# Performance work log

Hardware: AMD Instinct MI355X
Metric: run time of the kernel (lower is better)

Reference implementation:

```python
import jax, jax.numpy as jnp
import numpy as np

N_NODES = 100000
N_EDGES = 1600000
IN_DIM, HIDDEN, OUT = 256, 128, 64


def setup_inputs() -> dict:
    key = jax.random.key(0)
    k1, k2, k3, k4 = jax.random.split(key, 4)
    x = jax.random.normal(k1, (N_NODES, IN_DIM), dtype=jnp.float32)
    edge_index = jax.random.randint(k2, (2, N_EDGES), 0, N_NODES, dtype=jnp.int32)
    # glorot-ish init for the GCN linear layers
    W1 = jax.random.normal(k3, (IN_DIM, HIDDEN), dtype=jnp.float32) / np.sqrt(IN_DIM)
    b1 = jnp.zeros((HIDDEN,), dtype=jnp.float32)
    W2 = jax.random.normal(k4, (HIDDEN, OUT), dtype=jnp.float32) / np.sqrt(HIDDEN)
    b2 = jnp.zeros((OUT,), dtype=jnp.float32)
    return {"x": x, "edge_index": edge_index, "W1": W1, "b1": b1, "W2": W2, "b2": b2}


def gcn_layer(x, src, dst, W, b):
    """PyG GCNConv: add self-loops, symmetric deg^-1/2 normalization,
    linear transform, scatter-add aggregation, bias."""
    h = x @ W  # [N, F_out]
    # degree over self-looped graph: in-degree(dst counts) + 1 self loop
    deg = jax.ops.segment_sum(jnp.ones((src.shape[0],), h.dtype), dst,
                              num_segments=N_NODES) + 1.0
    dinv = jax.lax.rsqrt(deg)  # [N]
    coef = dinv[src] * dinv[dst]  # [E]
    agg = jax.ops.segment_sum(h[src] * coef[:, None], dst, num_segments=N_NODES)
    # self-loop contribution (norm = dinv[i]^2) without materializing loop edges
    agg = agg + h * (dinv * dinv)[:, None]
    return agg + b


def reference(x, edge_index, W1, b1, W2, b2):
    src, dst = edge_index[0], edge_index[1]
    h = jax.nn.relu(gcn_layer(x, src, dst, W1, b1))
    return jax.nn.relu(gcn_layer(h, src, dst, W2, b2))
```

## Files before the change

kernel.cpp:

```cpp
#include <hip/hip_runtime.h>

#define N_NODES 100000
#define N_EDGES 1600000
#define IN_DIM 256
#define HIDDEN 128
#define OUT_DIM 64

#define NBIN 391
#define NBLK3 256
#define CHUNK 6250
#define NMAT (NBIN * NBLK3)
#define NBLK_SCAN (NMAT / 256)
#define CAP 6144

#define G1_TILES 782
#define G_HIST  160
#define G_SCAN1 120
#define G_SCAN2 60
#define G_SCAT  160
#define G_FINE  282
#define OFF_HIST  0
#define OFF_SCAN1 160
#define OFF_SCAN2 280
#define OFF_SCAT  340
#define OFF_FINE  500

#define CAPL1 640
#define CAPL2 1024

typedef __bf16 bf16x8 __attribute__((ext_vector_type(8)));
typedef __bf16 bf16x4 __attribute__((ext_vector_type(4)));
typedef float f32x4 __attribute__((ext_vector_type(4)));

__device__ __forceinline__ int bsw1h(int c, int kk) {
    return c * 128 + (kk ^ ((c & 7) << 3));
}

__device__ __forceinline__ void gemm1_tile(const float* __restrict__ X,
                                           const float* __restrict__ W1,
                                           __bf16* __restrict__ H,
                                           int bid, __bf16* Bs) {
    const int t = threadIdx.x;
    const int wave = t >> 6;
    const int lane = t & 63;
    const int lm = lane & 15;
    const int q = lane >> 4;
    const int row0 = bid * 128;
    const int g = row0 + wave * 16 + lm;

    f32x4 acc[8] = {};

    for (int half = 0; half < 2; ++half) {
        __syncthreads();
        for (int p = 0; p < 4; ++p) {
            int i = t + 512 * p;
            int c = i & 127;
            int kg = i >> 7;
            float v[8];
            #pragma unroll
            for (int j = 0; j < 8; ++j)
                v[j] = W1[(half * 128 + kg * 8 + j) * HIDDEN + c];
            bf16x8 w;
            #pragma unroll
            for (int j = 0; j < 8; ++j) w[j] = (__bf16)v[j];
            *(bf16x8*)&Bs[bsw1h(c, kg * 8)] = w;
        }
        __syncthreads();

        #pragma unroll
        for (int k0 = 0; k0 < 128; k0 += 32) {
            float4 v0 = make_float4(0.f, 0.f, 0.f, 0.f), v1 = v0;
            if (g < N_NODES) {
                const float* p = &X[(size_t)g * IN_DIM + half * 128 + k0 + q * 8];
                v0 = *(const float4*)p;
                v1 = *(const float4*)(p + 4);
            }
            bf16x8 a;
            a[0] = (__bf16)v0.x; a[1] = (__bf16)v0.y;
            a[2] = (__bf16)v0.z; a[3] = (__bf16)v0.w;
            a[4] = (__bf16)v1.x; a[5] = (__bf16)v1.y;
            a[6] = (__bf16)v1.z; a[7] = (__bf16)v1.w;
            #pragma unroll
            for (int ni = 0; ni < 8; ++ni) {
                bf16x8 bfr = *(const bf16x8*)&Bs[bsw1h(ni * 16 + lm, k0 + q * 8)];
                acc[ni] = __builtin_amdgcn_mfma_f32_16x16x32_bf16(a, bfr, acc[ni], 0, 0, 0);
            }
        }
    }

    #pragma unroll
    for (int r = 0; r < 4; ++r) {
        int grow = row0 + wave * 16 + q * 4 + r;
        if (grow < N_NODES) {
            #pragma unroll
            for (int ni = 0; ni < 8; ++ni)
                H[grow * HIDDEN + ni * 16 + lm] = (__bf16)acc[ni][r];
        }
    }
}

__global__ __launch_bounds__(512, 4)
void k_hist_g(const int* __restrict__ dst, int* __restrict__ cnt2,
              const float* __restrict__ X, const float* __restrict__ W1,
              __bf16* __restrict__ H) {
    __shared__ __attribute__((aligned(16))) char smem[32768];
    if (blockIdx.x < NBLK3) {
        int* hist = (int*)smem;
        int t = threadIdx.x;
        for (int i = t; i < NBIN; i += 512) hist[i] = 0;
        __syncthreads();
        int base = blockIdx.x * CHUNK;
        for (int i = t; i < CHUNK; i += 512)
            atomicAdd(&hist[dst[base + i] >> 8], 1);
        __syncthreads();
        for (int k = t; k < NBIN; k += 512)
            cnt2[k * NBLK3 + blockIdx.x] = hist[k];
    } else {
        gemm1_tile(X, W1, H, OFF_HIST + (int)blockIdx.x - NBLK3, (__bf16*)smem);
    }
}

__global__ __launch_bounds__(512, 4)
void k_scan1_g(int* __restrict__ a, int* __restrict__ bsum,
               const float* __restrict__ X, const float* __restrict__ W1,
               __bf16* __restrict__ H) {
    __shared__ __attribute__((aligned(16))) char smem[32768];
    if (blockIdx.x < NBLK_SCAN) {
        int* tmp = (int*)smem;
        int t = threadIdx.x;
        int i = blockIdx.x * 256 + t;
        int v = 0;
        if (t < 256) { v = a[i]; tmp[t] = v; }
        __syncthreads();
        #pragma unroll
        for (int off = 1; off < 256; off <<= 1) {
            int p = (t >= off && t < 256) ? tmp[t - off] : 0;
            __syncthreads();
            if (t < 256) tmp[t] += p;
            __syncthreads();
        }
        if (t < 256) a[i] = tmp[t] - v;
        if (t == 255) bsum[blockIdx.x] = tmp[255];
    } else {
        gemm1_tile(X, W1, H, OFF_SCAN1 + (int)blockIdx.x - NBLK_SCAN, (__bf16*)smem);
    }
}

__global__ __launch_bounds__(512, 4)
void k_scan2_g(int* __restrict__ bsum,
               const float* __restrict__ X, const float* __restrict__ W1,
               __bf16* __restrict__ H) {
    __shared__ __attribute__((aligned(16))) char smem[32768];
    if (blockIdx.x == 0) {
        int* tmp = (int*)smem;
        int t = threadIdx.x;
        int v = (t < NBLK_SCAN) ? bsum[t] : 0;
        tmp[t] = v;
        __syncthreads();
        #pragma unroll
        for (int off = 1; off < 512; off <<= 1) {
            int p = (t >= off) ? tmp[t - off] : 0;
            __syncthreads();
            tmp[t] += p;
            __syncthreads();
        }
        if (t < NBLK_SCAN) bsum[t] = tmp[t] - v;
    } else {
        gemm1_tile(X, W1, H, OFF_SCAN2 + (int)blockIdx.x - 1, (__bf16*)smem);
    }
}

__global__ __launch_bounds__(512, 4)
void k_scatter_g(const int* __restrict__ src, const int* __restrict__ dst,
                 const int* __restrict__ off2, const int* __restrict__ bsum,
                 unsigned int* __restrict__ ebuf,
                 const float* __restrict__ X, const float* __restrict__ W1,
                 __bf16* __restrict__ H) {
    __shared__ __attribute__((aligned(16))) char smem[32768];
    if (blockIdx.x < NBLK3) {
        int* cursor = (int*)smem;
        int t = threadIdx.x;
        for (int k = t; k < NBIN; k += 512)
            cursor[k] = off2[k * NBLK3 + blockIdx.x] + bsum[k];
        __syncthreads();
        int base = blockIdx.x * CHUNK;
        for (int i = t; i < CHUNK; i += 512) {
            int s = src[base + i], d = dst[base + i];
            int pos = atomicAdd(&cursor[d >> 8], 1);
            ebuf[pos] = ((unsigned)s << 8) | (unsigned)(d & 255);
        }
    } else {
        gemm1_tile(X, W1, H, OFF_SCAT + (int)blockIdx.x - NBLK3, (__bf16*)smem);
    }
}

struct FineSm {
    int hist[256];
    int tmp[256];
    int nodeoff[256];
    int cursor[256];
    unsigned int ed[CAP];
    int sOut[CAP];
};

__global__ __launch_bounds__(512, 4)
void k_fine_g(const unsigned int* __restrict__ ebuf, const int* __restrict__ off2,
              const int* __restrict__ bsum,
              int* __restrict__ esrc, int* __restrict__ rowstart,
              float* __restrict__ dinv,
              const float* __restrict__ X, const float* __restrict__ W1,
              __bf16* __restrict__ H) {
    __shared__ __attribute__((aligned(16))) char smem[sizeof(FineSm)];
    if (blockIdx.x < NBIN) {
        FineSm* sm = (FineSm*)smem;
        const int k = blockIdx.x;
        const int t = threadIdx.x;
        const int e0 = off2[k * NBLK3] + bsum[k];
        const int e1 = (k + 1 < NBIN) ? off2[(k + 1) * NBLK3] + bsum[k + 1] : N_EDGES;
        int m = e1 - e0;
        if (m > CAP) m = CAP;

        if (t < 256) sm->hist[t] = 0;
        __syncthreads();
        for (int i = t; i < m; i += 512) {
            unsigned v = ebuf[e0 + i];
            sm->ed[i] = v;
            atomicAdd(&sm->hist[v & 255], 1);
        }
        __syncthreads();

        int v = (t < 256) ? sm->hist[t] : 0;
        if (t < 256) sm->tmp[t] = v;
        __syncthreads();
        #pragma unroll
        for (int off = 1; off < 256; off <<= 1) {
            int p = (t >= off && t < 256) ? sm->tmp[t - off] : 0;
            __syncthreads();
            if (t < 256) sm->tmp[t] += p;
            __syncthreads();
        }
        if (t < 256) {
            sm->nodeoff[t] = sm->tmp[t] - v;
            sm->cursor[t] = sm->tmp[t] - v;
        }
        __syncthreads();

        for (int i = t; i < m; i += 512) {
            unsigned e = sm->ed[i];
            int pos = atomicAdd(&sm->cursor[e & 255], 1);
            sm->sOut[pos] = (int)(e >> 8);
        }
        __syncthreads();

        for (int i = t; i < m; i += 512) esrc[e0 + i] = sm->sOut[i];

        if (t < 256) {
            int n = k * 256 + t;
            if (n < N_NODES) {
                rowstart[n] = e0 + sm->nodeoff[t];
                dinv[n] = rsqrtf((float)sm->hist[t] + 1.0f);
            }
        }
        if (k == 0 && t == 0) rowstart[N_NODES] = N_EDGES;
    } else {
        gemm1_tile(X, W1, H, OFF_FINE + (int)blockIdx.x - NBIN, (__bf16*)smem);
    }
}

__device__ __forceinline__ int bsw2(int c, int kk) {
    return c * 128 + (kk ^ ((c & 7) << 3));
}

__launch_bounds__(256)
__global__ void k_gather1f(const int* __restrict__ rowstart, const int* __restrict__ esrc,
                           const float* __restrict__ dinv,
                           const __bf16* __restrict__ H, const float* __restrict__ b1,
                           const float* __restrict__ W2,
                           __bf16* __restrict__ H2) {
    __shared__ int eidx[CAPL1];
    __shared__ __attribute__((aligned(16))) __bf16 As[16 * 128];
    __shared__ __attribute__((aligned(16))) __bf16 Bs[64 * 128];

    const int t = threadIdx.x;
    const int nb = blockIdx.x * 16;
    const int e0 = rowstart[nb];
    const int m = rowstart[nb + 16] - e0;

    #pragma unroll
    for (int p = 0; p < 4; ++p) {
        int i = t + 256 * p;
        int c = i & 63;
        int kg = i >> 6;
        float v[8];
        #pragma unroll
        for (int jj = 0; jj < 8; ++jj)
            v[jj] = W2[(kg * 8 + jj) * OUT_DIM + c];
        bf16x8 w;
        #pragma unroll
        for (int jj = 0; jj < 8; ++jj) w[jj] = (__bf16)v[jj];
        *(bf16x8*)&Bs[bsw2(c, kg * 8)] = w;
    }
    for (int i = t; i < m && i < CAPL1; i += 256) eidx[i] = esrc[e0 + i];
    __syncthreads();

    const int nl = t >> 4;
    const int n = nb + nl;
    const int jc = t & 15;
    const int j = jc * 8;

    float dn = dinv[n];
    float s = dn * dn;
    bf16x8 h = *(const bf16x8*)&H[n * HIDDEN + j];
    float acc[8];
    #pragma unroll
    for (int i = 0; i < 8; ++i) acc[i] = (float)h[i] * s;

    int p = rowstart[n] - e0, p1 = rowstart[n + 1] - e0;
    if (p1 <= CAPL1) {
        for (; p + 3 < p1; p += 4) {
            int s0 = eidx[p + 0], s1 = eidx[p + 1], s2 = eidx[p + 2], s3 = eidx[p + 3];
            float c0 = dinv[s0] * dn, c1 = dinv[s1] * dn;
            float c2 = dinv[s2] * dn, c3 = dinv[s3] * dn;
            bf16x8 v0 = *(const bf16x8*)&H[s0 * HIDDEN + j];
            bf16x8 v1 = *(const bf16x8*)&H[s1 * HIDDEN + j];
            bf16x8 v2 = *(const bf16x8*)&H[s2 * HIDDEN + j];
            bf16x8 v3 = *(const bf16x8*)&H[s3 * HIDDEN + j];
            #pragma unroll
            for (int i = 0; i < 8; ++i) acc[i] = fmaf((float)v0[i], c0, acc[i]);
            #pragma unroll
            for (int i = 0; i < 8; ++i) acc[i] = fmaf((float)v1[i], c1, acc[i]);
            #pragma unroll
            for (int i = 0; i < 8; ++i) acc[i] = fmaf((float)v2[i], c2, acc[i]);
            #pragma unroll
            for (int i = 0; i < 8; ++i) acc[i] = fmaf((float)v3[i], c3, acc[i]);
        }
        for (; p < p1; ++p) {
            int sidx = eidx[p];
            float c = dinv[sidx] * dn;
            bf16x8 v = *(const bf16x8*)&H[sidx * HIDDEN + j];
            #pragma unroll
            for (int i = 0; i < 8; ++i) acc[i] = fmaf((float)v[i], c, acc[i]);
        }
    } else {
        const int* ep = esrc + e0;
        for (; p + 3 < p1; p += 4) {
            int s0 = ep[p + 0], s1 = ep[p + 1], s2 = ep[p + 2], s3 = ep[p + 3];
            float c0 = dinv[s0] * dn, c1 = dinv[s1] * dn;
            float c2 = dinv[s2] * dn, c3 = dinv[s3] * dn;
            bf16x8 v0 = *(const bf16x8*)&H[s0 * HIDDEN + j];
            bf16x8 v1 = *(const bf16x8*)&H[s1 * HIDDEN + j];
            bf16x8 v2 = *(const bf16x8*)&H[s2 * HIDDEN + j];
            bf16x8 v3 = *(const bf16x8*)&H[s3 * HIDDEN + j];
            #pragma unroll
            for (int i = 0; i < 8; ++i) acc[i] = fmaf((float)v0[i], c0, acc[i]);
            #pragma unroll
            for (int i = 0; i < 8; ++i) acc[i] = fmaf((float)v1[i], c1, acc[i]);
            #pragma unroll
            for (int i = 0; i < 8; ++i) acc[i] = fmaf((float)v2[i], c2, acc[i]);
            #pragma unroll
            for (int i = 0; i < 8; ++i) acc[i] = fmaf((float)v3[i], c3, acc[i]);
        }
        for (; p < p1; ++p) {
            int sidx = ep[p];
            float c = dinv[sidx] * dn;
            bf16x8 v = *(const bf16x8*)&H[sidx * HIDDEN + j];
            #pragma unroll
            for (int i = 0; i < 8; ++i) acc[i] = fmaf((float)v[i], c, acc[i]);
        }
    }

    float4 bb0 = *(const float4*)&b1[j];
    float4 bb1 = *(const float4*)&b1[j + 4];
    bf16x8 o;
    o[0] = (__bf16)fmaxf(acc[0] + bb0.x, 0.f);
    o[1] = (__bf16)fmaxf(acc[1] + bb0.y, 0.f);
    o[2] = (__bf16)fmaxf(acc[2] + bb0.z, 0.f);
    o[3] = (__bf16)fmaxf(acc[3] + bb0.w, 0.f);
    o[4] = (__bf16)fmaxf(acc[4] + bb1.x, 0.f);
    o[5] = (__bf16)fmaxf(acc[5] + bb1.y, 0.f);
    o[6] = (__bf16)fmaxf(acc[6] + bb1.z, 0.f);
    o[7] = (__bf16)fmaxf(acc[7] + bb1.w, 0.f);
    *(bf16x8*)&As[nl * 128 + (jc ^ (nl & 7)) * 8] = o;
    __syncthreads();

    const int wave = t >> 6;
    const int lane = t & 63;
    const int lm = lane & 15;
    const int q = lane >> 4;

    f32x4 acc2 = {};
    #pragma unroll
    for (int k0 = 0; k0 < HIDDEN; k0 += 32) {
        int c = (k0 >> 3) + q;
        bf16x8 a = *(const bf16x8*)&As[lm * 128 + (c ^ (lm & 7)) * 8];
        bf16x8 bfr = *(const bf16x8*)&Bs[bsw2(wave * 16 + lm, k0 + q * 8)];
        acc2 = __builtin_amdgcn_mfma_f32_16x16x32_bf16(a, bfr, acc2, 0, 0, 0);
    }
    #pragma unroll
    for (int r = 0; r < 4; ++r)
        H2[(nb + q * 4 + r) * OUT_DIM + wave * 16 + lm] = (__bf16)acc2[r];
}

__launch_bounds__(256)
__global__ void k_gather2(const int* __restrict__ rowstart, const int* __restrict__ esrc,
                          const float* __restrict__ dinv,
                          const __bf16* __restrict__ H2, const float* __restrict__ b2,
                          float* __restrict__ OUT) {
    __shared__ int eidx[CAPL2];
    const int nb = blockIdx.x * 32;
    const int t = threadIdx.x;
    const int e0 = rowstart[nb];
    const int m = rowstart[nb + 32] - e0;
    for (int i = t; i < m && i < CAPL2; i += 256) eidx[i] = esrc[e0 + i];
    __syncthreads();

    const int n = nb + (t >> 3);
    const int j = (t & 7) * 8;

    float dn = dinv[n];
    float s = dn * dn;
    bf16x8 h = *(const bf16x8*)&H2[n * OUT_DIM + j];
    float acc[8];
    #pragma unroll
    for (int i = 0; i < 8; ++i) acc[i] = (float)h[i] * s;

    int p = rowstart[n] - e0, p1 = rowstart[n + 1] - e0;
    if (p1 <= CAPL2) {
        for (; p + 3 < p1; p += 4) {
            int s0 = eidx[p + 0], s1 = eidx[p + 1], s2 = eidx[p + 2], s3 = eidx[p + 3];
            float c0 = dinv[s0] * dn, c1 = dinv[s1] * dn;
            float c2 = dinv[s2] * dn, c3 = dinv[s3] * dn;
            bf16x8 v0 = *(const bf16x8*)&H2[s0 * OUT_DIM + j];
            bf16x8 v1 = *(const bf16x8*)&H2[s1 * OUT_DIM + j];
            bf16x8 v2 = *(const bf16x8*)&H2[s2 * OUT_DIM + j];
            bf16x8 v3 = *(const bf16x8*)&H2[s3 * OUT_DIM + j];
            #pragma unroll
            for (int i = 0; i < 8; ++i) acc[i] = fmaf((float)v0[i], c0, acc[i]);
            #pragma unroll
            for (int i = 0; i < 8; ++i) acc[i] = fmaf((float)v1[i], c1, acc[i]);
            #pragma unroll
            for (int i = 0; i < 8; ++i) acc[i] = fmaf((float)v2[i], c2, acc[i]);
            #pragma unroll
            for (int i = 0; i < 8; ++i) acc[i] = fmaf((float)v3[i], c3, acc[i]);
        }
        for (; p < p1; ++p) {
            int sidx = eidx[p];
            float c = dinv[sidx] * dn;
            bf16x8 v = *(const bf16x8*)&H2[sidx * OUT_DIM + j];
            #pragma unroll
            for (int i = 0; i < 8; ++i) acc[i] = fmaf((float)v[i], c, acc[i]);
        }
    } else {
        const int* ep = esrc + e0;
        for (; p + 3 < p1; p += 4) {
            int s0 = ep[p + 0], s1 = ep[p + 1], s2 = ep[p + 2], s3 = ep[p + 3];
            float c0 = dinv[s0] * dn, c1 = dinv[s1] * dn;
            float c2 = dinv[s2] * dn, c3 = dinv[s3] * dn;
            bf16x8 v0 = *(const bf16x8*)&H2[s0 * OUT_DIM + j];
            bf16x8 v1 = *(const bf16x8*)&H2[s1 * OUT_DIM + j];
            bf16x8 v2 = *(const bf16x8*)&H2[s2 * OUT_DIM + j];
            bf16x8 v3 = *(const bf16x8*)&H2[s3 * OUT_DIM + j];
            #pragma unroll
            for (int i = 0; i < 8; ++i) acc[i] = fmaf((float)v0[i], c0, acc[i]);
            #pragma unroll
            for (int i = 0; i < 8; ++i) acc[i] = fmaf((float)v1[i], c1, acc[i]);
            #pragma unroll
            for (int i = 0; i < 8; ++i) acc[i] = fmaf((float)v2[i], c2, acc[i]);
            #pragma unroll
            for (int i = 0; i < 8; ++i) acc[i] = fmaf((float)v3[i], c3, acc[i]);
        }
        for (; p < p1; ++p) {
            int sidx = ep[p];
            float c = dinv[sidx] * dn;
            bf16x8 v = *(const bf16x8*)&H2[sidx * OUT_DIM + j];
            #pragma unroll
            for (int i = 0; i < 8; ++i) acc[i] = fmaf((float)v[i], c, acc[i]);
        }
    }

    float4 bb0 = *(const float4*)&b2[j];
    float4 bb1 = *(const float4*)&b2[j + 4];
    float4 o0, o1;
    o0.x = fmaxf(acc[0] + bb0.x, 0.f);
    o0.y = fmaxf(acc[1] + bb0.y, 0.f);
    o0.z = fmaxf(acc[2] + bb0.z, 0.f);
    o0.w = fmaxf(acc[3] + bb0.w, 0.f);
    o1.x = fmaxf(acc[4] + bb1.x, 0.f);
    o1.y = fmaxf(acc[5] + bb1.y, 0.f);
    o1.z = fmaxf(acc[6] + bb1.z, 0.f);
    o1.w = fmaxf(acc[7] + bb1.w, 0.f);
    *(float4*)&OUT[n * OUT_DIM + j] = o0;
    *(float4*)&OUT[n * OUT_DIM + j + 4] = o1;
}

extern "C" void kernel_launch(void* const* d_in, const int* in_sizes, int n_in,
                              void* d_out, int out_size, void* d_ws, size_t ws_size,
                              hipStream_t stream) {
    const float* x  = (const float*)d_in[0];
    const int* ei   = (const int*)d_in[1];
    const float* W1 = (const float*)d_in[2];
    const float* b1 = (const float*)d_in[3];
    const float* W2 = (const float*)d_in[4];
    const float* b2 = (const float*)d_in[5];
    float* out = (float*)d_out;

    const int* src = ei;
    const int* dst = ei + N_EDGES;

    char* ws = (char*)d_ws;
    int*          cnt2     = (int*)         (ws + 0x000000);
    int*          bsum     = (int*)         (ws + 0x080000);
    int*          rowstart = (int*)         (ws + 0x090000);
    float*        dinv     = (float*)       (ws + 0x100000);
    unsigned int* ebuf     = (unsigned int*)(ws + 0x180000);
    int*          esrc     = (int*)         (ws + 0x800000);
    __bf16*       h1       = (__bf16*)      (ws + 0xE80000);
    __bf16*       h2       = (__bf16*)      (ws + 0x4280000);

    k_hist_g   <<<NBLK3     + G_HIST,  512, 0, stream>>>(dst, cnt2, x, W1, h1);
    k_scan1_g  <<<NBLK_SCAN + G_SCAN1, 512, 0, stream>>>(cnt2, bsum, x, W1, h1);
    k_scan2_g  <<<1         + G_SCAN2, 512, 0, stream>>>(bsum, x, W1, h1);
    k_scatter_g<<<NBLK3     + G_SCAT,  512, 0, stream>>>(src, dst, cnt2, bsum, ebuf,
                                                         x, W1, h1);
    k_fine_g   <<<NBIN      + G_FINE,  512, 0, stream>>>(ebuf, cnt2, bsum, esrc,
                                                         rowstart, dinv, x, W1, h1);

    k_gather1f<<<N_NODES / 16, 256, 0, stream>>>(rowstart, esrc, dinv, h1, b1, W2, h2);
    k_gather2<<<N_NODES / 32, 256, 0, stream>>>(rowstart, esrc, dinv, h2, b2, out);
}
```

Baseline: 320.7 us.

## Remove scan2 launch and stage scatter through shared memory for coalesced writes

Drops the separate second-level scan kernel. Each scatter block now redoes the small bsum prefix scan locally, and each fine block sums the preceding bsum entries to find its edge range. The scatter step now builds a local per-bin histogram, sorts its chunk into shared memory, and writes it out to ebuf in bin-contiguous runs, replacing random global stores. GEMM tile counts are redistributed across the remaining kernels. The cost is more shared memory per block (launch bounds lowered to 3), redundant scans in every block, and a serial per-bin fill loop for binof.

```diff
diff --git a/kernel.cpp b/kernel.cpp
--- a/kernel.cpp
+++ b/kernel.cpp
@@ -13,16 +13,13 @@
 #define NBLK_SCAN (NMAT / 256)
 #define CAP 6144
 
-#define G1_TILES 782
-#define G_HIST  160
-#define G_SCAN1 120
-#define G_SCAN2 60
-#define G_SCAT  160
+#define G_HIST  180
+#define G_SCAN1 140
+#define G_SCAT  180
 #define G_FINE  282
 #define OFF_HIST  0
-#define OFF_SCAN1 160
-#define OFF_SCAN2 280
-#define OFF_SCAT  340
+#define OFF_SCAN1 180
+#define OFF_SCAT  320
 #define OFF_FINE  500
 
 #define CAPL1 640
@@ -146,48 +143,72 @@
     }
 }
 
-__global__ __launch_bounds__(512, 4)
-void k_scan2_g(int* __restrict__ bsum,
-               const float* __restrict__ X, const float* __restrict__ W1,
-               __bf16* __restrict__ H) {
-    __shared__ __attribute__((aligned(16))) char smem[32768];
-    if (blockIdx.x == 0) {
-        int* tmp = (int*)smem;
-        int t = threadIdx.x;
-        int v = (t < NBLK_SCAN) ? bsum[t] : 0;
-        tmp[t] = v;
-        __syncthreads();
-        #pragma unroll
-        for (int off = 1; off < 512; off <<= 1) {
-            int p = (t >= off) ? tmp[t - off] : 0;
-            __syncthreads();
-            tmp[t] += p;
-            __syncthreads();
-        }
-        if (t < NBLK_SCAN) bsum[t] = tmp[t] - v;
-    } else {
-        gemm1_tile(X, W1, H, OFF_SCAN2 + (int)blockIdx.x - 1, (__bf16*)smem);
-    }
-}
-
-__global__ __launch_bounds__(512, 4)
+struct ScatSm {
+    int bscan[392];
+    int hist[392];
+    int base[392];
+    int curs[392];
+    unsigned short binof[CHUNK];
+    unsigned int sOut[CHUNK];
+};
+
+__global__ __launch_bounds__(512, 3)
 void k_scatter_g(const int* __restrict__ src, const int* __restrict__ dst,
                  const int* __restrict__ off2, const int* __restrict__ bsum,
                  unsigned int* __restrict__ ebuf,
                  const float* __restrict__ X, const float* __restrict__ W1,
                  __bf16* __restrict__ H) {
-    __shared__ __attribute__((aligned(16))) char smem[32768];
+    __shared__ __attribute__((aligned(16))) char smem[sizeof(ScatSm)];
     if (blockIdx.x < NBLK3) {
-        int* cursor = (int*)smem;
-        int t = threadIdx.x;
+        ScatSm* sm = (ScatSm*)smem;
+        const int t = threadIdx.x;
+        const int b = blockIdx.x;
+        int* tmp = (int*)sm->sOut;
+
+        int v = (t < NBIN) ? bsum[t] : 0;
+        tmp[t] = v;
+        __syncthreads();
+        #pragma unroll
+        for (int off = 1; off < 512; off <<= 1) {
+            int p = (t >= off) ? tmp[t - off] : 0;
+            __syncthreads();
+            tmp[t] += p;
+            __syncthreads();
+        }
+        if (t < NBIN) sm->bscan[t] = tmp[t] - v;
+        if (t < NBIN) sm->hist[t] = 0;
+        __syncthreads();
+        const int ebase = b * CHUNK;
+        for (int i = t; i < CHUNK; i += 512)
+            atomicAdd(&sm->hist[dst[ebase + i] >> 8], 1);
+        __syncthreads();
+        int hv = (t < NBIN) ? sm->hist[t] : 0;
+        tmp[t] = hv;
+        __syncthreads();
+        #pragma unroll
+        for (int off = 1; off < 512; off <<= 1) {
+            int p = (t >= off) ? tmp[t - off] : 0;
+            __syncthreads();
+            tmp[t] += p;
+            __syncthreads();
+        }
+        if (t < NBIN) { sm->base[t] = tmp[t] - hv; sm->curs[t] = tmp[t] - hv; }
+        if (t == 0) sm->base[NBIN] = CHUNK;
+        __syncthreads();
         for (int k = t; k < NBIN; k += 512)
-            cursor[k] = off2[k * NBLK3 + blockIdx.x] + bsum[k];
-        __syncthreads();
-        int base = blockIdx.x * CHUNK;
+            for (int idx = sm->base[k]; idx < sm->base[k + 1]; ++idx)
+                sm->binof[idx] = (unsigned short)k;
+        __syncthreads();
         for (int i = t; i < CHUNK; i += 512) {
-            int s = src[base + i], d = dst[base + i];
-            int pos = atomicAdd(&cursor[d >> 8], 1);
-            ebuf[pos] = ((unsigned)s << 8) | (unsigned)(d & 255);
+            int s = src[ebase + i], d = dst[ebase + i];
+            int pos = atomicAdd(&sm->curs[d >> 8], 1);
+            sm->sOut[pos] = ((unsigned)s << 8) | (unsigned)(d & 255);
+        }
+        __syncthreads();
+        for (int i = t; i < CHUNK; i += 512) {
+            int k = sm->binof[i];
+            int gpos = off2[k * NBLK3 + b] + sm->bscan[k] + (i - sm->base[k]);
+            ebuf[gpos] = sm->sOut[i];
         }
     } else {
         gemm1_tile(X, W1, H, OFF_SCAT + (int)blockIdx.x - NBLK3, (__bf16*)smem);
@@ -204,8 +225,7 @@
 };
 
 __global__ __launch_bounds__(512, 4)
-void k_fine_g(const unsigned int* __restrict__ ebuf, const int* __restrict__ off2,
-              const int* __restrict__ bsum,
+void k_fine_g(const unsigned int* __restrict__ ebuf, const int* __restrict__ bsum,
               int* __restrict__ esrc, int* __restrict__ rowstart,
               float* __restrict__ dinv,
               const float* __restrict__ X, const float* __restrict__ W1,
@@ -215,10 +235,18 @@
         FineSm* sm = (FineSm*)smem;
         const int k = blockIdx.x;
         const int t = threadIdx.x;
-        const int e0 = off2[k * NBLK3] + bsum[k];
-        const int e1 = (k + 1 < NBIN) ? off2[(k + 1) * NBLK3] + bsum[k + 1] : N_EDGES;
+
+        if (t == 0) sm->tmp[0] = 0;
+        __syncthreads();
+        int part = 0;
+        for (int i = t; i < k; i += 512) part += bsum[i];
+        if (part) atomicAdd(&sm->tmp[0], part);
+        __syncthreads();
+        const int e0 = sm->tmp[0];
+        const int e1 = (k + 1 < NBIN) ? e0 + bsum[k] : N_EDGES;
         int m = e1 - e0;
         if (m > CAP) m = CAP;
+        __syncthreads();
 
         if (t < 256) sm->hist[t] = 0;
         __syncthreads();
@@ -519,10 +547,9 @@
 
     k_hist_g   <<<NBLK3     + G_HIST,  512, 0, stream>>>(dst, cnt2, x, W1, h1);
     k_scan1_g  <<<NBLK_SCAN + G_SCAN1, 512, 0, stream>>>(cnt2, bsum, x, W1, h1);
-    k_scan2_g  <<<1         + G_SCAN2, 512, 0, stream>>>(bsum, x, W1, h1);
     k_scatter_g<<<NBLK3     + G_SCAT,  512, 0, stream>>>(src, dst, cnt2, bsum, ebuf,
                                                          x, W1, h1);
-    k_fine_g   <<<NBIN      + G_FINE,  512, 0, stream>>>(ebuf, cnt2, bsum, esrc,
+    k_fine_g   <<<NBIN      + G_FINE,  512, 0, stream>>>(ebuf, bsum, esrc,
                                                          rowstart, dinv, x, W1, h1);
 
     k_gather1f<<<N_NODES / 16, 256, 0, stream>>>(rowstart, esrc, dinv, h1, b1, W2, h2);
```

New measurement: 306.4 us. 4.5% less time.
